# Kernel optimization log

Hardware: AMD Instinct MI355X
Metric: run time of the kernel (lower is better)

## Reference

```python
import jax, jax.numpy as jnp
import numpy as np

NUM_ORI = 4
VM_R, VM_RG = 10.0, 15.0
B_INH, G_INH = 1.5, 1.0
VM_W, VM_W2 = 0.1, 0.4
VM_WG, VM_W2G = 0.2, 0.4
BORDER_K = 11   # int(10*1.1)=11, already odd
GROUP_K = 23    # int(15*1.5)=22 -> +1 to make odd


def create_von_mises(size, r0, theta0, centered, w, w2):
    x = np.arange(size) - size / 2
    y = -(np.arange(size) - size / 2)
    X, Y = np.meshgrid(x, y)
    if centered:
        X = X + r0 * np.cos(theta0)
        Y = Y + r0 * np.sin(theta0)
    r = np.sqrt(X ** 2 + Y ** 2)
    th = np.arctan2(Y, X)
    # np.i0 == scipy.special.iv(0, .) for real args (I0 is even)
    return np.exp(r0 * w * np.cos(th - theta0)) / np.i0(w2 * (r - r0))


def make_filters():
    borders, groups = [], []
    for ori in np.arange(0.0, 180.0, 180.0 / NUM_ORI):
        a = ori * np.pi / 180.0
        b = (ori + 180.0) * np.pi / 180.0
        borders.append(create_von_mises(BORDER_K, VM_R, a, True, VM_W, VM_W2))
        borders.append(create_von_mises(BORDER_K, VM_R, b, True, VM_W, VM_W2))
        g1 = create_von_mises(GROUP_K, VM_RG, a, False, VM_W, VM_W2)
        g2 = create_von_mises(GROUP_K, VM_RG, b, False, VM_WG, VM_W2G)
        groups += [g1, g1, g2, g2]
    # only border filters are normalized to [-1, 1] in the original code
    borders = [f / (f.max() / 2.0) - 1.0 for f in borders]
    Wb = np.stack(borders)[:, None].astype(np.float32)   # [2*O, 1, 11, 11]
    Wg = np.stack(groups)[:, None].astype(np.float32)    # [4*O, 1, 23, 23]
    return jnp.asarray(Wb), jnp.asarray(Wg)


def setup_inputs() -> dict:
    key = jax.random.key(0)
    inp = jax.random.uniform(key, (4, 2, 512, 512), dtype=jnp.float32)
    Wb, Wg = make_filters()
    return {"inp": inp, "W_border": Wb, "W_group": Wg}


def _conv(x, w, pad, groups):
    return jax.lax.conv_general_dilated(
        x, w, (1, 1), [(pad, pad), (pad, pad)],
        dimension_numbers=("NCHW", "OIHW", "NCHW"),
        feature_group_count=groups)


def _spike(v):
    # LIF with tau_mem=0.01, zero initial v_mem, single step: alpha=exp(-1/tau)~0,
    # so v_mem = input; spike when v_mem >= threshold (1.0).
    return (v >= 1.0).astype(v.dtype)


def reference(inp, W_border, W_group):
    B, _, H, W = inp.shape
    pad_b = (BORDER_K - 1) // 2
    pad_g = (GROUP_K - 1) // 2
    # border ownership: conv each polarity with the 8 von-Mises filters + LIF
    pos = _spike(_conv(inp[:, 0:1], W_border, pad_b, 1))  # [B, 2*O, H, W]
    neg = _spike(_conv(inp[:, 1:2], W_border, pad_b, 1))
    vmap_ = inp.sum(1)[:, None]                           # [B, 1, H, W]
    pe, po = pos[:, 0::2], pos[:, 1::2]   # even=ori, odd=opposite ori
    ne, no = neg[:, 0::2], neg[:, 1::2]
    b13 = _spike(vmap_ * (pe - no * B_INH)) + _spike(vmap_ * (ne - po * B_INH))
    b24 = _spike(vmap_ * (po - ne * B_INH)) + _spike(vmap_ * (no - pe * B_INH))
    # winner-take-all over orientations
    diff = b13 - b24                                      # [B, O, H, W]
    tp = jnp.abs(diff)
    wta = jax.lax.stop_gradient(
        (tp == tp.max(axis=1, keepdims=True)).astype(inp.dtype))
    b1p = _spike(wta * diff)
    b1n = _spike(-(wta * diff))
    # channel order is ori-major: [t1_o, t2_o, t3_o, t4_o] per orientation
    border = jnp.stack(
        [b1p * b13, b1p * b24 * G_INH, b1n * b24, b1n * b13 * G_INH],
        axis=2).reshape(B, 4 * NUM_ORI, H, W)
    g = _spike(_conv(border, W_group, pad_g, 4 * NUM_ORI))
    g = g.reshape(B, NUM_ORI, 4, H, W)
    return (_spike(g[:, :, 0] - g[:, :, 1])
            + _spike(g[:, :, 2] - g[:, :, 3])).sum(1)     # [B, H, W]
```

## Files before the change

### kernel.cpp

```cpp
#include <hip/hip_runtime.h>

#define HH 512
#define WW 512
#define NB 4

#define K1 11
#define PAD1 5
#define T1X 32
#define T1Y 16
#define IN1X 42
#define IN1Y 26
#define S1 44

__device__ __forceinline__ unsigned conv8_pass2(const float* __restrict__ sm,
                                                const float* __restrict__ Wb,
                                                int py, int px)
{
    float acc[8][2];
    #pragma unroll
    for (int c = 0; c < 8; c++) { acc[c][0] = 0.f; acc[c][1] = 0.f; }

    #pragma unroll 1
    for (int ky = 0; ky < K1; ky++) {
        const float2* rp = (const float2*)&sm[(py + ky) * S1 + px];
        float a[12];
        #pragma unroll
        for (int r = 0; r < 6; r++) *(float2*)&a[2 * r] = rp[r];
        #pragma unroll
        for (int c = 0; c < 8; c++) {
            #pragma unroll
            for (int kx = 0; kx < K1; kx++) {
                const float wv = Wb[c * 121 + ky * 11 + kx];
                acc[c][0] = fmaf(a[kx],     wv, acc[c][0]);
                acc[c][1] = fmaf(a[kx + 1], wv, acc[c][1]);
            }
        }
    }
    unsigned bits = 0;
    #pragma unroll
    for (int c = 0; c < 8; c++) {
        bits |= (acc[c][0] >= 1.f ? 1u : 0u) << (c * 2);
        bits |= (acc[c][1] >= 1.f ? 1u : 0u) << (c * 2 + 1);
    }
    return bits;
}

__global__ __launch_bounds__(256, 8) void stage1_kernel(
    const float* __restrict__ inp, const float* __restrict__ Wb,
    unsigned char* __restrict__ border)
{
    __shared__ __align__(16) float s0[IN1Y * S1];
    __shared__ __align__(16) float s1[IN1Y * S1];

    const int b   = blockIdx.z;
    const int tx0 = blockIdx.x * T1X;
    const int ty0 = blockIdx.y * T1Y;
    const float* in0 = inp + ((size_t)b * 2 + 0) * (HH * WW);
    const float* in1 = inp + ((size_t)b * 2 + 1) * (HH * WW);

    for (int i = threadIdx.x; i < IN1Y * IN1X; i += 256) {
        int iy = i / IN1X, ix = i - iy * IN1X;
        int gy = ty0 + iy - PAD1, gx = tx0 + ix - PAD1;
        bool ok = (gy >= 0) & (gy < HH) & (gx >= 0) & (gx < WW);
        int idx = gy * WW + gx;
        s0[iy * S1 + ix] = ok ? in0[idx] : 0.f;
        s1[iy * S1 + ix] = ok ? in1[idx] : 0.f;
    }
    __syncthreads();

    const int lx = threadIdx.x & 15;
    const int ly = threadIdx.x >> 4;
    const int px = lx * 2;
    const int py = ly;

    const unsigned bitP = conv8_pass2(s0, Wb, py, px);
    const unsigned bitN = conv8_pass2(s1, Wb, py, px);

    const int gy = ty0 + py;
    const int gxbase = tx0 + px;

    float vm[2];
    #pragma unroll
    for (int p = 0; p < 2; p++)
        vm[p] = s0[(py + PAD1) * S1 + px + PAD1 + p]
              + s1[(py + PAD1) * S1 + px + PAD1 + p];

    float b13[4][2], b24[4][2];
    #pragma unroll
    for (int o = 0; o < 4; o++) {
        #pragma unroll
        for (int p = 0; p < 2; p++) {
            float pe = (float)((bitP >> (4 * o + p))     & 1u);
            float po = (float)((bitP >> (4 * o + 2 + p)) & 1u);
            float ne = (float)((bitN >> (4 * o + p))     & 1u);
            float no = (float)((bitN >> (4 * o + 2 + p)) & 1u);
            float sa = (vm[p] * (pe - 1.5f * no) >= 1.f) ? 1.f : 0.f;
            float sb = (vm[p] * (ne - 1.5f * po) >= 1.f) ? 1.f : 0.f;
            b13[o][p] = sa + sb;
            float sc = (vm[p] * (po - 1.5f * ne) >= 1.f) ? 1.f : 0.f;
            float sd = (vm[p] * (no - 1.5f * pe) >= 1.f) ? 1.f : 0.f;
            b24[o][p] = sc + sd;
        }
    }
    float mxp[2];
    #pragma unroll
    for (int p = 0; p < 2; p++) {
        float m = 0.f;
        #pragma unroll
        for (int o = 0; o < 4; o++) m = fmaxf(m, fabsf(b13[o][p] - b24[o][p]));
        mxp[p] = m;
    }
    #pragma unroll
    for (int o = 0; o < 4; o++) {
        unsigned short w0 = 0, w1 = 0, w2 = 0, w3 = 0;
        #pragma unroll
        for (int p = 0; p < 2; p++) {
            float d   = b13[o][p] - b24[o][p];
            float wta = (fabsf(d) == mxp[p]) ? 1.f : 0.f;
            float b1p = (wta * d >= 1.f)    ? 1.f : 0.f;
            float b1n = (-(wta * d) >= 1.f) ? 1.f : 0.f;
            w0 |= (unsigned short)(unsigned char)(b1p * b13[o][p]) << (8 * p);
            w1 |= (unsigned short)(unsigned char)(b1p * b24[o][p]) << (8 * p);
            w2 |= (unsigned short)(unsigned char)(b1n * b24[o][p]) << (8 * p);
            w3 |= (unsigned short)(unsigned char)(b1n * b13[o][p]) << (8 * p);
        }
        size_t base = (((size_t)b * 16 + 4 * o) * HH + gy) * WW + gxbase;
        *(unsigned short*)&border[base]                       = w0;
        *(unsigned short*)&border[base + (size_t)HH * WW]     = w1;
        *(unsigned short*)&border[base + (size_t)2 * HH * WW] = w2;
        *(unsigned short*)&border[base + (size_t)3 * HH * WW] = w3;
    }
}

#define K2 23
#define PAD2 11
#define T2X 32
#define T2Y 512
#define SROW 18
#define R2 534

__device__ __forceinline__ float ubyte_f(unsigned dw, int byi) {
    return (float)((dw >> (8 * byi)) & 0xffu);
}

__device__ __forceinline__ void s2_load(const unsigned* __restrict__ tile,
                                        int trow, int lx, unsigned d[8])
{
    const uint2* tp2 = (const uint2*)&tile[trow * SROW + 2 * lx];
    #pragma unroll
    for (int r2 = 0; r2 < 4; r2++) {
        uint2 v = tp2[r2];
        d[2 * r2] = v.x; d[2 * r2 + 1] = v.y;
    }
}

__device__ __forceinline__ void s2_cvt(const unsigned d[8], float a[31])
{
    #pragma unroll
    for (int j = 1; j <= 30; j++) a[j] = ubyte_f(d[j >> 2], j & 3);
}

__global__ __launch_bounds__(256, 4) void stage2_kernel(
    const unsigned char* __restrict__ border, const float* __restrict__ Wg,
    unsigned char* __restrict__ gsp)
{
    __shared__ unsigned tile[R2 * SROW];

    const int z   = blockIdx.z;
    const int b   = z >> 4;
    const int c   = z & 15;
    const int tx0 = blockIdx.x * T2X;
    const unsigned char* bp = border + ((size_t)b * 16 + c) * (HH * WW);

    for (int i = threadIdx.x; i < R2 * 16; i += 256) {
        int iy = i >> 4, cc = i & 15;
        int gy  = iy - PAD2;
        int gx0 = tx0 - 12 + 4 * cc;
        unsigned u = 0;
        if (((unsigned)gy < HH) & ((unsigned)gx0 < WW))
            u = *(const unsigned*)(bp + (size_t)gy * WW + gx0);
        tile[iy * SROW + cc] = u;
    }
    __syncthreads();

    const int lx = threadIdx.x & 3;
    const int ly = threadIdx.x >> 2;
    const int px = lx * 8;
    const int py = ly * 8;

    float acc[8][8];
    #pragma unroll
    for (int dy = 0; dy < 8; dy++)
        #pragma unroll
        for (int p = 0; p < 8; p++) acc[dy][p] = 0.f;

    const float* wc = Wg + c * (K2 * K2);

    unsigned dc[8];
    s2_load(tile, py + 0, lx, dc);

    #pragma unroll 1
    for (int t = 0; t < 7; t++) {
        float a[31];
        s2_cvt(dc, a);
        s2_load(tile, py + t + 1, lx, dc);
        #pragma unroll
        for (int dy = 0; dy < 8; dy++) {
            if (t - dy >= 0) {
                const float* wr = wc + (t - dy) * K2;
                #pragma unroll
                for (int kx = 0; kx < K2; kx++) {
                    const float wv = wr[kx];
                    #pragma unroll
                    for (int p = 0; p < 8; p++)
                        acc[dy][p] = fmaf(a[p + kx + 1], wv, acc[dy][p]);
                }
            }
        }
    }

    #pragma unroll 1
    for (int t = 7; t < 23; t++) {
        float a[31];
        s2_cvt(dc, a);
        s2_load(tile, py + t + 1, lx, dc);
        const float* w0 = wc + t * K2;
        #pragma unroll
        for (int kx = 0; kx < K2; kx++) {
            float wv[8];
            #pragma unroll
            for (int d = 0; d < 8; d++) wv[d] = w0[kx - 23 * d];
            #pragma unroll
            for (int p = 0; p < 8; p++) {
                const float av = a[p + kx + 1];
                #pragma unroll
                for (int d = 0; d < 8; d++)
                    acc[d][p] = fmaf(av, wv[d], acc[d][p]);
            }
        }
    }

    #pragma unroll 1
    for (int t = 23; t < 29; t++) {
        float a[31];
        s2_cvt(dc, a);
        s2_load(tile, py + t + 1, lx, dc);
        #pragma unroll
        for (int dy = 0; dy < 8; dy++) {
            if (t - dy < K2) {
                const float* wr = wc + (t - dy) * K2;
                #pragma unroll
                for (int kx = 0; kx < K2; kx++) {
                    const float wv = wr[kx];
                    #pragma unroll
                    for (int p = 0; p < 8; p++)
                        acc[dy][p] = fmaf(a[p + kx + 1], wv, acc[dy][p]);
                }
            }
        }
    }
    {
        float a[31];
        s2_cvt(dc, a);
        const float* wr = wc + 22 * K2;
        #pragma unroll
        for (int kx = 0; kx < K2; kx++) {
            const float wv = wr[kx];
            #pragma unroll
            for (int p = 0; p < 8; p++)
                acc[7][p] = fmaf(a[p + kx + 1], wv, acc[7][p]);
        }
    }

    const int ox = tx0 + px;
    unsigned char* gp = gsp + ((size_t)b * 16 + c) * (HH * WW);
    #pragma unroll
    for (int dy = 0; dy < 8; dy++) {
        const int oy = py + dy;
        unsigned lo = 0, hi = 0;
        #pragma unroll
        for (int p = 0; p < 4; p++) lo |= (acc[dy][p]     >= 1.f ? 1u : 0u) << (8 * p);
        #pragma unroll
        for (int p = 0; p < 4; p++) hi |= (acc[dy][p + 4] >= 1.f ? 1u : 0u) << (8 * p);
        uint2 v; v.x = lo; v.y = hi;
        *(uint2*)&gp[(size_t)oy * WW + ox] = v;
    }
}

__global__ __launch_bounds__(256) void combine_kernel(
    const unsigned char* __restrict__ gsp, float* __restrict__ out)
{
    const int idx = blockIdx.x * 256 + threadIdx.x;
    const int b = idx >> 16;
    const int r = idx & 65535;
    const unsigned* g = (const unsigned*)gsp;
    const int pb = b * 16;
    unsigned s = 0;
    #pragma unroll
    for (int o = 0; o < 4; o++) {
        unsigned g0 = g[(size_t)(pb + 4 * o + 0) * 65536 + r];
        unsigned g1 = g[(size_t)(pb + 4 * o + 1) * 65536 + r];
        unsigned g2 = g[(size_t)(pb + 4 * o + 2) * 65536 + r];
        unsigned g3 = g[(size_t)(pb + 4 * o + 3) * 65536 + r];
        s += ((g0 & ~g1) & 0x01010101u) + ((g2 & ~g3) & 0x01010101u);
    }
    float4 f;
    f.x = (float)(s & 255u);
    f.y = (float)((s >> 8) & 255u);
    f.z = (float)((s >> 16) & 255u);
    f.w = (float)(s >> 24);
    ((float4*)out)[idx] = f;
}

extern "C" void kernel_launch(void* const* d_in, const int* in_sizes, int n_in,
                              void* d_out, int out_size, void* d_ws, size_t ws_size,
                              hipStream_t stream)
{
    const float* inp = (const float*)d_in[0];
    const float* Wb  = (const float*)d_in[1];
    const float* Wg  = (const float*)d_in[2];
    unsigned char* border = (unsigned char*)d_ws;
    unsigned char* gsp    = border + (size_t)NB * 16 * HH * WW;
    float* out = (float*)d_out;

    dim3 blk(256);
    dim3 g1(WW / T1X, HH / T1Y, NB);
    stage1_kernel<<<g1, blk, 0, stream>>>(inp, Wb, border);
    dim3 g2(WW / T2X, 1, NB * 16);
    stage2_kernel<<<g2, blk, 0, stream>>>(border, Wg, gsp);
    dim3 g3((NB * HH * WW / 4) / 256);
    combine_kernel<<<g3, blk, 0, stream>>>(gsp, out);
}
```

Measured before the change: 272.0 us.

## Compute four pixels per thread and fuse both polarity convolutions in stage one

Stage one now uses 32x32 tiles, with each thread computing four horizontally adjacent pixels for both input polarities in a single loop. Each weight load is shared by eight FMAs, and the per-row shared-memory reads are amortized. The shared-memory halo overhead per output also drops. In exchange, register usage grows to 64 accumulators, occupancy is reduced via launch bounds, and outputs are written as 32-bit stores.

After: 264.3 us (median of 3 runs). 1.03x faster.

```diff
diff --git a/kernel.cpp b/kernel.cpp
--- a/kernel.cpp
+++ b/kernel.cpp
@@ -7,50 +7,16 @@
 #define K1 11
 #define PAD1 5
 #define T1X 32
-#define T1Y 16
-#define IN1X 42
-#define IN1Y 26
-#define S1 44
-
-__device__ __forceinline__ unsigned conv8_pass2(const float* __restrict__ sm,
-                                                const float* __restrict__ Wb,
-                                                int py, int px)
-{
-    float acc[8][2];
-    #pragma unroll
-    for (int c = 0; c < 8; c++) { acc[c][0] = 0.f; acc[c][1] = 0.f; }
-
-    #pragma unroll 1
-    for (int ky = 0; ky < K1; ky++) {
-        const float2* rp = (const float2*)&sm[(py + ky) * S1 + px];
-        float a[12];
-        #pragma unroll
-        for (int r = 0; r < 6; r++) *(float2*)&a[2 * r] = rp[r];
-        #pragma unroll
-        for (int c = 0; c < 8; c++) {
-            #pragma unroll
-            for (int kx = 0; kx < K1; kx++) {
-                const float wv = Wb[c * 121 + ky * 11 + kx];
-                acc[c][0] = fmaf(a[kx],     wv, acc[c][0]);
-                acc[c][1] = fmaf(a[kx + 1], wv, acc[c][1]);
-            }
-        }
-    }
-    unsigned bits = 0;
-    #pragma unroll
-    for (int c = 0; c < 8; c++) {
-        bits |= (acc[c][0] >= 1.f ? 1u : 0u) << (c * 2);
-        bits |= (acc[c][1] >= 1.f ? 1u : 0u) << (c * 2 + 1);
-    }
-    return bits;
-}
-
-__global__ __launch_bounds__(256, 8) void stage1_kernel(
+#define T1Y 32
+#define IN1 42
+#define S1B 44
+
+__global__ __launch_bounds__(256, 4) void stage1_kernel(
     const float* __restrict__ inp, const float* __restrict__ Wb,
     unsigned char* __restrict__ border)
 {
-    __shared__ __align__(16) float s0[IN1Y * S1];
-    __shared__ __align__(16) float s1[IN1Y * S1];
+    __shared__ __align__(16) float s0[IN1 * S1B];
+    __shared__ __align__(16) float s1[IN1 * S1B];
 
     const int b   = blockIdx.z;
     const int tx0 = blockIdx.x * T1X;
@@ -58,42 +24,69 @@
     const float* in0 = inp + ((size_t)b * 2 + 0) * (HH * WW);
     const float* in1 = inp + ((size_t)b * 2 + 1) * (HH * WW);
 
-    for (int i = threadIdx.x; i < IN1Y * IN1X; i += 256) {
-        int iy = i / IN1X, ix = i - iy * IN1X;
+    for (int i = threadIdx.x; i < IN1 * IN1; i += 256) {
+        int iy = i / IN1, ix = i - iy * IN1;
         int gy = ty0 + iy - PAD1, gx = tx0 + ix - PAD1;
         bool ok = (gy >= 0) & (gy < HH) & (gx >= 0) & (gx < WW);
         int idx = gy * WW + gx;
-        s0[iy * S1 + ix] = ok ? in0[idx] : 0.f;
-        s1[iy * S1 + ix] = ok ? in1[idx] : 0.f;
+        s0[iy * S1B + ix] = ok ? in0[idx] : 0.f;
+        s1[iy * S1B + ix] = ok ? in1[idx] : 0.f;
     }
     __syncthreads();
 
-    const int lx = threadIdx.x & 15;
-    const int ly = threadIdx.x >> 4;
-    const int px = lx * 2;
-    const int py = ly;
-
-    const unsigned bitP = conv8_pass2(s0, Wb, py, px);
-    const unsigned bitN = conv8_pass2(s1, Wb, py, px);
-
-    const int gy = ty0 + py;
-    const int gxbase = tx0 + px;
-
-    float vm[2];
-    #pragma unroll
-    for (int p = 0; p < 2; p++)
-        vm[p] = s0[(py + PAD1) * S1 + px + PAD1 + p]
-              + s1[(py + PAD1) * S1 + px + PAD1 + p];
-
-    float b13[4][2], b24[4][2];
+    const int lx  = threadIdx.x & 7;
+    const int ly  = threadIdx.x >> 3;
+    const int px0 = lx * 4;
+    const int py  = ly;
+
+    float accP[8][4], accN[8][4];
+    #pragma unroll
+    for (int c = 0; c < 8; c++)
+        #pragma unroll
+        for (int p = 0; p < 4; p++) { accP[c][p] = 0.f; accN[c][p] = 0.f; }
+
+    #pragma unroll 1
+    for (int ky = 0; ky < K1; ky++) {
+        float a0[14], a1[14];
+        const float2* r0 = (const float2*)&s0[(py + ky) * S1B + px0];
+        const float2* r1 = (const float2*)&s1[(py + ky) * S1B + px0];
+        #pragma unroll
+        for (int r = 0; r < 7; r++) {
+            *(float2*)&a0[2 * r] = r0[r];
+            *(float2*)&a1[2 * r] = r1[r];
+        }
+        #pragma unroll
+        for (int c = 0; c < 8; c++) {
+            #pragma unroll
+            for (int kx = 0; kx < K1; kx++) {
+                const float wv = Wb[c * 121 + ky * 11 + kx];
+                #pragma unroll
+                for (int p = 0; p < 4; p++) {
+                    accP[c][p] = fmaf(a0[kx + p], wv, accP[c][p]);
+                    accN[c][p] = fmaf(a1[kx + p], wv, accN[c][p]);
+                }
+            }
+        }
+    }
+
+    const int gy  = ty0 + py;
+    const int gxb = tx0 + px0;
+
+    float vm[4];
+    #pragma unroll
+    for (int p = 0; p < 4; p++)
+        vm[p] = s0[(py + PAD1) * S1B + px0 + PAD1 + p]
+              + s1[(py + PAD1) * S1B + px0 + PAD1 + p];
+
+    float b13[4][4], b24[4][4];
     #pragma unroll
     for (int o = 0; o < 4; o++) {
         #pragma unroll
-        for (int p = 0; p < 2; p++) {
-            float pe = (float)((bitP >> (4 * o + p))     & 1u);
-            float po = (float)((bitP >> (4 * o + 2 + p)) & 1u);
-            float ne = (float)((bitN >> (4 * o + p))     & 1u);
-            float no = (float)((bitN >> (4 * o + 2 + p)) & 1u);
+        for (int p = 0; p < 4; p++) {
+            float pe = (accP[2 * o    ][p] >= 1.f) ? 1.f : 0.f;
+            float po = (accP[2 * o + 1][p] >= 1.f) ? 1.f : 0.f;
+            float ne = (accN[2 * o    ][p] >= 1.f) ? 1.f : 0.f;
+            float no = (accN[2 * o + 1][p] >= 1.f) ? 1.f : 0.f;
             float sa = (vm[p] * (pe - 1.5f * no) >= 1.f) ? 1.f : 0.f;
             float sb = (vm[p] * (ne - 1.5f * po) >= 1.f) ? 1.f : 0.f;
             b13[o][p] = sa + sb;
@@ -102,9 +95,9 @@
             b24[o][p] = sc + sd;
         }
     }
-    float mxp[2];
-    #pragma unroll
-    for (int p = 0; p < 2; p++) {
+    float mxp[4];
+    #pragma unroll
+    for (int p = 0; p < 4; p++) {
         float m = 0.f;
         #pragma unroll
         for (int o = 0; o < 4; o++) m = fmaxf(m, fabsf(b13[o][p] - b24[o][p]));
@@ -112,23 +105,23 @@
     }
     #pragma unroll
     for (int o = 0; o < 4; o++) {
-        unsigned short w0 = 0, w1 = 0, w2 = 0, w3 = 0;
-        #pragma unroll
-        for (int p = 0; p < 2; p++) {
+        unsigned w0 = 0, w1 = 0, w2 = 0, w3 = 0;
+        #pragma unroll
+        for (int p = 0; p < 4; p++) {
             float d   = b13[o][p] - b24[o][p];
             float wta = (fabsf(d) == mxp[p]) ? 1.f : 0.f;
             float b1p = (wta * d >= 1.f)    ? 1.f : 0.f;
             float b1n = (-(wta * d) >= 1.f) ? 1.f : 0.f;
-            w0 |= (unsigned short)(unsigned char)(b1p * b13[o][p]) << (8 * p);
-            w1 |= (unsigned short)(unsigned char)(b1p * b24[o][p]) << (8 * p);
-            w2 |= (unsigned short)(unsigned char)(b1n * b24[o][p]) << (8 * p);
-            w3 |= (unsigned short)(unsigned char)(b1n * b13[o][p]) << (8 * p);
-        }
-        size_t base = (((size_t)b * 16 + 4 * o) * HH + gy) * WW + gxbase;
-        *(unsigned short*)&border[base]                       = w0;
-        *(unsigned short*)&border[base + (size_t)HH * WW]     = w1;
-        *(unsigned short*)&border[base + (size_t)2 * HH * WW] = w2;
-        *(unsigned short*)&border[base + (size_t)3 * HH * WW] = w3;
+            w0 |= (unsigned)(unsigned char)(b1p * b13[o][p]) << (8 * p);
+            w1 |= (unsigned)(unsigned char)(b1p * b24[o][p]) << (8 * p);
+            w2 |= (unsigned)(unsigned char)(b1n * b24[o][p]) << (8 * p);
+            w3 |= (unsigned)(unsigned char)(b1n * b13[o][p]) << (8 * p);
+        }
+        size_t base = (((size_t)b * 16 + 4 * o) * HH + gy) * WW + gxb;
+        *(unsigned*)&border[base]                       = w0;
+        *(unsigned*)&border[base + (size_t)HH * WW]     = w1;
+        *(unsigned*)&border[base + (size_t)2 * HH * WW] = w2;
+        *(unsigned*)&border[base + (size_t)3 * HH * WW] = w3;
     }
 }
 
```
